# Kernel tuning notes

Hardware: AMD Instinct MI355X
Metric: run time of the kernel (lower is better)

Reference implementation:

```python
import jax, jax.numpy as jnp
import numpy as np


def setup_inputs() -> dict:
    key = jax.random.key(0)
    k1, k2, k3, k4, k5 = jax.random.split(key, 5)
    B, H, N, D = 32, 16, 1024, 128  # batch, heads, max_n_codes, head_dim
    transformer_t_1 = jax.random.normal(k1, (B, H, N, D), dtype=jnp.float32)
    transformer_t = jax.random.normal(k2, (B, H, N, D), dtype=jnp.float32)
    # valid-prefix padding vectors: first L entries nonzero, remainder zero
    lengths = jax.random.randint(k3, (B,), N // 2, N + 1)
    padding_t = (jnp.arange(N)[None, :] < lengths[:, None]).astype(jnp.int32)
    concat_w = jax.random.normal(k4, (1, 2 * D), dtype=jnp.float32) / np.sqrt(2 * D)
    concat_b = jax.random.normal(k5, (1,), dtype=jnp.float32) * 0.01
    return {
        "transformer_t_1": transformer_t_1,
        "transformer_t": transformer_t,
        "padding_t": padding_t,
        "max_n_codes": N,
        "concat_w": concat_w,
        "concat_b": concat_b,
    }


def reference(transformer_t_1, transformer_t, padding_t, max_n_codes, concat_w, concat_b):
    N = max_n_codes
    D = transformer_t.shape[-1]
    # create_padding_matrix: padd = index of first zero in padding row (else N);
    # mask positions n >= padd (True = masked out)
    iszero = padding_t == 0                      # [B, N]
    first0 = jnp.argmax(iszero, axis=1)          # [B]
    padd = jnp.where(iszero.any(axis=1), first0, N)
    mask = (jnp.arange(N)[None, :] >= padd[:, None])[:, None, :]  # [B, 1, N] -> bcast over heads

    # all_nodes_t_1: sum over node dim, broadcast back to every node
    s = transformer_t_1.sum(axis=2)              # [B, H, D]
    # concat Linear([all_nodes, transformer_t]) -> split weight into two halves
    w1 = concat_w[0, :D]
    w2 = concat_w[0, D:]
    score = (jnp.einsum('bhd,d->bh', s, w1)[:, :, None]
             + jnp.einsum('bhnd,d->bhn', transformer_t, w2)
             + concat_b[0])                      # [B, H, N]

    logits = jnp.where(mask, -jnp.inf, score)
    attn = jax.nn.softmax(logits, axis=-1)
    attn = jnp.where(mask, jnp.array(0.0, attn.dtype), attn)

    return transformer_t * attn[..., None] + transformer_t
```

## Files before the change

kernel.cpp:

```cpp
#include <hip/hip_runtime.h>

#define BB 32
#define HH 16
#define NN 1024
#define DD 128

__global__ __launch_bounds__(1024) void fused_kernel(const float* __restrict__ t,
                                                     const int* __restrict__ padding,
                                                     const float* __restrict__ w2,
                                                     float* __restrict__ out) {
    const int bh   = blockIdx.x;
    const int b    = bh >> 4;
    const int tid  = threadIdx.x;
    const int wid  = tid >> 6;
    const int lane = tid & 63;

    __shared__ float s_fac[NN];
    __shared__ int   red_i[16];
    __shared__ float red_f[16];

    const float* trow = t + (long)bh * NN * DD;

    int lm = (padding[b * NN + tid] == 0) ? tid : NN;
#pragma unroll
    for (int off = 32; off; off >>= 1) lm = min(lm, __shfl_xor(lm, off));
    if (lane == 0) red_i[wid] = lm;

    const int hw = tid >> 5;
    const int l  = tid & 31;
    const float4 wv = ((const float4*)w2)[l];
    const float4* rowp = (const float4*)(trow + (long)(hw * 32) * DD);

    float4 cur[4], nxt[4];
#pragma unroll
    for (int j = 0; j < 4; ++j) cur[j] = rowp[j * 32 + l];

#pragma unroll
    for (int g = 0; g < 8; ++g) {
        if (g < 7) {
#pragma unroll
            for (int j = 0; j < 4; ++j) nxt[j] = rowp[(g + 1) * 128 + j * 32 + l];
        }
        float p[4];
#pragma unroll
        for (int j = 0; j < 4; ++j)
            p[j] = cur[j].x * wv.x + cur[j].y * wv.y + cur[j].z * wv.z + cur[j].w * wv.w;

#pragma unroll
        for (int pr = 0; pr < 2; ++pr) {
            const float a = p[2 * pr], bq = p[2 * pr + 1];
            float x = (l < 16) ? a : bq;
            float y = (l < 16) ? bq : a;
            x += __shfl_xor(y, 16);
            x += __shfl_xor(x, 8);
            x += __shfl_xor(x, 4);
            x += __shfl_xor(x, 2);
            x += __shfl_xor(x, 1);
            const int n = hw * 32 + g * 4 + 2 * pr;
            if (l == 0)  s_fac[n]     = x;
            if (l == 16) s_fac[n + 1] = x;
        }
        if (g < 7) {
#pragma unroll
            for (int j = 0; j < 4; ++j) cur[j] = nxt[j];
        }
    }
    __syncthreads();

    int padd = NN;
#pragma unroll
    for (int k = 0; k < 16; ++k) padd = min(padd, red_i[k]);

    const float sc  = s_fac[tid];
    const float NEG = -3.4e38f;
    float m = (tid < padd) ? sc : NEG;
#pragma unroll
    for (int off = 32; off; off >>= 1) m = fmaxf(m, __shfl_xor(m, off));
    if (lane == 0) red_f[wid] = m;
    __syncthreads();
    float M = NEG;
#pragma unroll
    for (int k = 0; k < 16; ++k) M = fmaxf(M, red_f[k]);
    __syncthreads();

    const float e = (tid < padd) ? __expf(sc - M) : 0.f;
    float s = e;
#pragma unroll
    for (int off = 32; off; off >>= 1) s += __shfl_xor(s, off);
    if (lane == 0) red_f[wid] = s;
    __syncthreads();
    float S = 0.f;
#pragma unroll
    for (int k = 0; k < 16; ++k) S += red_f[k];

    const float inv = (S > 0.f) ? (1.0f / S) : 0.f;
    s_fac[tid] = 1.f + e * inv;
    __syncthreads();

    const float4* t4 = (const float4*)trow;
    float4*       o4 = (float4*)(out + (long)bh * NN * DD);
#pragma unroll 8
    for (int it = 0; it < 32; ++it) {
        const int i4 = it * 1024 + tid;
        const float f = s_fac[i4 >> 5];
        float4 v = t4[i4];
        v.x *= f; v.y *= f; v.z *= f; v.w *= f;
        o4[i4] = v;
    }
}

extern "C" void kernel_launch(void* const* d_in, const int* in_sizes, int n_in,
                              void* d_out, int out_size, void* d_ws, size_t ws_size,
                              hipStream_t stream) {
    const float* t       = (const float*)d_in[1];
    const int*   padding = (const int*)d_in[2];
    const float* cw      = (const float*)d_in[4];
    float*       out     = (float*)d_out;

    fused_kernel<<<BB * HH, 1024, 0, stream>>>(t, padding, cw + DD, out);
}
```

Measured before the change: 584.2 us.

## Keep each thread's row slice in registers to avoid re-reading input

Each thread now loads all 32 float4 values of its 32-row slice into registers once, computes the dot-product scores from them, and reuses the same registers for the final scaled output write. This removes the second global read of the whole transformer_t tile, cutting HBM traffic from two reads plus one write to one read plus one write. In exchange each thread holds 128 extra floats in registers at 1024 threads per block, which risks spilling or limiting occupancy, and all loads are issued up front instead of being double-buffered.

```diff
diff --git a/kernel.cpp b/kernel.cpp
--- a/kernel.cpp
+++ b/kernel.cpp
@@ -31,39 +31,26 @@
     const float4 wv = ((const float4*)w2)[l];
     const float4* rowp = (const float4*)(trow + (long)(hw * 32) * DD);
 
-    float4 cur[4], nxt[4];
+    float4 v[32];
 #pragma unroll
-    for (int j = 0; j < 4; ++j) cur[j] = rowp[j * 32 + l];
+    for (int k = 0; k < 32; ++k) v[k] = rowp[k * 32 + l];
 
 #pragma unroll
-    for (int g = 0; g < 8; ++g) {
-        if (g < 7) {
-#pragma unroll
-            for (int j = 0; j < 4; ++j) nxt[j] = rowp[(g + 1) * 128 + j * 32 + l];
-        }
-        float p[4];
-#pragma unroll
-        for (int j = 0; j < 4; ++j)
-            p[j] = cur[j].x * wv.x + cur[j].y * wv.y + cur[j].z * wv.z + cur[j].w * wv.w;
-
-#pragma unroll
-        for (int pr = 0; pr < 2; ++pr) {
-            const float a = p[2 * pr], bq = p[2 * pr + 1];
-            float x = (l < 16) ? a : bq;
-            float y = (l < 16) ? bq : a;
-            x += __shfl_xor(y, 16);
-            x += __shfl_xor(x, 8);
-            x += __shfl_xor(x, 4);
-            x += __shfl_xor(x, 2);
-            x += __shfl_xor(x, 1);
-            const int n = hw * 32 + g * 4 + 2 * pr;
-            if (l == 0)  s_fac[n]     = x;
-            if (l == 16) s_fac[n + 1] = x;
-        }
-        if (g < 7) {
-#pragma unroll
-            for (int j = 0; j < 4; ++j) cur[j] = nxt[j];
-        }
+    for (int pr = 0; pr < 16; ++pr) {
+        const float a  = v[2 * pr].x     * wv.x + v[2 * pr].y     * wv.y
+                       + v[2 * pr].z     * wv.z + v[2 * pr].w     * wv.w;
+        const float bq = v[2 * pr + 1].x * wv.x + v[2 * pr + 1].y * wv.y
+                       + v[2 * pr + 1].z * wv.z + v[2 * pr + 1].w * wv.w;
+        float x = (l < 16) ? a : bq;
+        float y = (l < 16) ? bq : a;
+        x += __shfl_xor(y, 16);
+        x += __shfl_xor(x, 8);
+        x += __shfl_xor(x, 4);
+        x += __shfl_xor(x, 2);
+        x += __shfl_xor(x, 1);
+        const int n = hw * 32 + 2 * pr;
+        if (l == 0)  s_fac[n]     = x;
+        if (l == 16) s_fac[n + 1] = x;
     }
     __syncthreads();
 
@@ -97,15 +84,13 @@
     s_fac[tid] = 1.f + e * inv;
     __syncthreads();
 
-    const float4* t4 = (const float4*)trow;
-    float4*       o4 = (float4*)(out + (long)bh * NN * DD);
-#pragma unroll 8
-    for (int it = 0; it < 32; ++it) {
-        const int i4 = it * 1024 + tid;
-        const float f = s_fac[i4 >> 5];
-        float4 v = t4[i4];
-        v.x *= f; v.y *= f; v.z *= f; v.w *= f;
-        o4[i4] = v;
+    float4* o4row = (float4*)(out + (long)bh * NN * DD + (long)(hw * 32) * DD);
+#pragma unroll
+    for (int k = 0; k < 32; ++k) {
+        const float f = s_fac[hw * 32 + k];
+        float4 w = v[k];
+        w.x *= f; w.y *= f; w.z *= f; w.w *= f;
+        o4row[k * 32 + l] = w;
     }
 }
 
```

After: 632.0 us. 1.08x slower.
